# Performance work log

Hardware: AMD Instinct MI355X
Metric: run time of the kernel (lower is better)

## Reference

```python
import jax, jax.numpy as jnp
import numpy as np

VOXEL_DIM = (64, 64, 64)
VOXEL_SIZE = 0.04
STRIDE = 4.0  # backbone2d_stride


def setup_inputs() -> dict:
    key = jax.random.key(0)
    k1, k2 = jax.random.split(key, 2)
    bs, nv, cin, h, w = 4, 12, 384, 64, 64
    cout = 32
    vit_feats = jax.random.normal(k1, (bs, nv, cin, h, w), dtype=jnp.float32)
    w_reduce = jax.random.normal(k2, (cout, cin), dtype=jnp.float32) * 0.05
    b_reduce = jnp.zeros((cout,), dtype=jnp.float32)
    # Realistic pinhole projections: K @ [I | t], camera ~3m from grid center.
    rng = np.random.default_rng(0)
    f, cx, cy = 128.0, 128.0, 128.0
    K = np.array([[f, 0.0, cx], [0.0, f, cy], [0.0, 0.0, 1.0]])
    projs = np.zeros((bs, nv, 3, 4), dtype=np.float32)
    for v in range(nv):
        t = np.array([0.2 * rng.standard_normal(), 0.2 * rng.standard_normal(),
                      3.0 + 0.3 * rng.standard_normal()])
        E = np.concatenate([np.eye(3), t[:, None]], axis=1)  # 3x4
        projs[:, v] = (K @ E).astype(np.float32)
    return {"vit_feats": vit_feats, "w_reduce": w_reduce,
            "b_reduce": b_reduce, "projection": jnp.asarray(projs)}


def _backproject(proj, feats):
    """proj: (b,3,4), feats: (b,c,h,w) -> volume (b,c,N), valid (b,N)."""
    nx, ny, nz = VOXEL_DIM
    N = nx * ny * nz
    b, c, h, w = feats.shape
    X, Y, Z = jnp.meshgrid(jnp.arange(nx), jnp.arange(ny), jnp.arange(nz), indexing='ij')
    coords = jnp.stack([X.ravel(), Y.ravel(), Z.ravel()]).astype(feats.dtype)  # (3, N)
    origin = jnp.array([[-nx * VOXEL_SIZE / 2],
                        [-ny * VOXEL_SIZE / 2],
                        [-nz * VOXEL_SIZE / 2]], dtype=feats.dtype)
    world = coords * VOXEL_SIZE + origin                    # (3, N)
    world = jnp.concatenate([world, jnp.ones((1, N), feats.dtype)], axis=0)  # (4, N)
    cam = jnp.einsum('bij,jn->bin', proj, world)            # (b, 3, N)
    px = jnp.round(cam[:, 0] / cam[:, 2]).astype(jnp.int32)
    py = jnp.round(cam[:, 1] / cam[:, 2]).astype(jnp.int32)
    pz = cam[:, 2]
    valid = (px >= 0) & (py >= 0) & (px < w) & (py < h) & (pz > 0)  # (b, N)
    pxc = jnp.clip(px, 0, w - 1)
    pyc = jnp.clip(py, 0, h - 1)
    # per-batch gather: feats[b, :, py, px]
    gath = jax.vmap(lambda f, yy, xx: f[:, yy, xx])(feats, pyc, pxc)  # (b, c, N)
    vol = jnp.where(valid[:, None, :], gath, jnp.zeros((), feats.dtype))
    return vol, valid


def reference(vit_feats, w_reduce, b_reduce, projection):
    bs, nv, cin, h, w = vit_feats.shape
    cout = w_reduce.shape[0]
    nx, ny, nz = VOXEL_DIM
    N = nx * ny * nz
    # 1x1 conv channel reduction
    feats = jnp.einsum('bnchw,oc->bnohw', vit_feats, w_reduce) \
            + b_reduce[None, None, :, None, None]
    # divide intrinsics rows by the 2D backbone stride
    proj = projection.at[:, :, :2, :].set(projection[:, :, :2, :] / STRIDE)
    feats_v = jnp.moveaxis(feats, 1, 0)   # (nv, b, c, h, w)
    proj_v = jnp.moveaxis(proj, 1, 0)     # (nv, b, 3, 4)

    def step(carry, xs):
        vol, cnt = carry
        p, f = xs
        v, m = _backproject(p, f)
        return (vol + v, cnt + m.astype(vol.dtype)), None

    vol0 = jnp.zeros((bs, cout, N), jnp.float32)
    cnt0 = jnp.zeros((bs, N), jnp.float32)
    (vol, cnt), _ = jax.lax.scan(step, (vol0, cnt0), (proj_v, feats_v))
    # volume / valid, zeroed where never observed
    cnt_b = cnt[:, None, :]
    out = jnp.where(cnt_b > 0, vol / jnp.maximum(cnt_b, 1.0), jnp.zeros((), vol.dtype))
    return out.reshape(bs, cout, nx, ny, nz)
```

## Files before the change

kernel.cpp:

```cpp
#include <hip/hip_runtime.h>

#define NV 12
#define CIN 384
#define COUT 32
#define HW 4096
#define NVOX 262144
#define KSTEPS 12
#define KSTEP 32
#define KPAD 33
#define PIXB 64

typedef __attribute__((ext_vector_type(8))) short short8v;
typedef __attribute__((ext_vector_type(4))) short short4v;
typedef __attribute__((ext_vector_type(4))) float f32x4;

__device__ __forceinline__ short bf16b(float x) {
    union { float f; unsigned u; } c; c.f = x;
    unsigned r = (c.u + 0x7fffu + ((c.u >> 16) & 1u)) >> 16;
    return (short)r;
}

__global__ __launch_bounds__(256) void w_prep_kernel(
    const float* __restrict__ w, short* __restrict__ wfrag)
{
    const int t = blockIdx.x * 256 + threadIdx.x;
    if (t >= 48 * 32) return;
    const int sg = t >> 5, o = t & 31;
    const int s = sg >> 2, g = sg & 3;
    short8v v;
#pragma unroll
    for (int i = 0; i < 8; ++i)
        v[i] = bf16b(w[o * CIN + s * 32 + g * 8 + i]);
    *reinterpret_cast<short8v*>(wfrag + t * 8) = v;
}

__global__ __launch_bounds__(256) void mv_reduce_mfma_kernel(
    const float* __restrict__ vit, const short* __restrict__ wfrag,
    const float* __restrict__ bias, short* __restrict__ feats)
{
    __shared__ float lds[PIXB][KPAD];

    const int bid  = blockIdx.x;
    const int bv   = bid >> 6;
    const int pix0 = (bid & 63) * PIXB;

    const int tid  = threadIdx.x;
    const int wave = tid >> 6;
    const int l    = tid & 63;
    const int col  = l & 15;
    const int g    = l >> 4;

    const int kk  = tid >> 4;
    const int px4 = (tid & 15) * 4;

    const float* vbase = vit + (size_t)bv * CIN * HW + pix0;
    const short8v* wf  = reinterpret_cast<const short8v*>(wfrag);

    f32x4 acc0 = {0.f, 0.f, 0.f, 0.f};
    f32x4 acc1 = {0.f, 0.f, 0.f, 0.f};

#pragma unroll
    for (int s = 0; s < KSTEPS; ++s) {
        const float4 r0 = *reinterpret_cast<const float4*>(
            vbase + (size_t)(s * KSTEP + kk) * HW + px4);
        const float4 r1 = *reinterpret_cast<const float4*>(
            vbase + (size_t)(s * KSTEP + kk + 16) * HW + px4);

        __syncthreads();
        lds[px4 + 0][kk] = r0.x;  lds[px4 + 1][kk] = r0.y;
        lds[px4 + 2][kk] = r0.z;  lds[px4 + 3][kk] = r0.w;
        lds[px4 + 0][kk + 16] = r1.x;  lds[px4 + 1][kk + 16] = r1.y;
        lds[px4 + 2][kk + 16] = r1.z;  lds[px4 + 3][kk + 16] = r1.w;
        __syncthreads();

        const float4 f0 = *reinterpret_cast<const float4*>(&lds[wave * 16 + col][8 * g]);
        const float4 f1 = *reinterpret_cast<const float4*>(&lds[wave * 16 + col][8 * g + 4]);

        short8v bfr;
        bfr[0] = bf16b(f0.x); bfr[1] = bf16b(f0.y);
        bfr[2] = bf16b(f0.z); bfr[3] = bf16b(f0.w);
        bfr[4] = bf16b(f1.x); bfr[5] = bf16b(f1.y);
        bfr[6] = bf16b(f1.z); bfr[7] = bf16b(f1.w);

        const short8v a0 = wf[(s * 4 + g) * 32 + col];
        const short8v a1 = wf[(s * 4 + g) * 32 + 16 + col];

        acc0 = __builtin_amdgcn_mfma_f32_16x16x32_bf16(a0, bfr, acc0, 0, 0, 0);
        acc1 = __builtin_amdgcn_mfma_f32_16x16x32_bf16(a1, bfr, acc1, 0, 0, 0);
    }

    short* dst = feats + ((size_t)bv * HW + pix0 + wave * 16 + col) * COUT;
    const float4 b0 = *reinterpret_cast<const float4*>(bias + 4 * g);
    const float4 b1 = *reinterpret_cast<const float4*>(bias + 16 + 4 * g);
    short4v o0, o1;
    o0[0] = bf16b(acc0[0] + b0.x); o0[1] = bf16b(acc0[1] + b0.y);
    o0[2] = bf16b(acc0[2] + b0.z); o0[3] = bf16b(acc0[3] + b0.w);
    o1[0] = bf16b(acc1[0] + b1.x); o1[1] = bf16b(acc1[1] + b1.y);
    o1[2] = bf16b(acc1[2] + b1.z); o1[3] = bf16b(acc1[3] + b1.w);
    *reinterpret_cast<short4v*>(dst + 4 * g) = o0;
    *reinterpret_cast<short4v*>(dst + 16 + 4 * g) = o1;
}

__global__ __launch_bounds__(256) void mv_fuse_kernel(
    const unsigned short* __restrict__ feats, const float* __restrict__ proj,
    float* __restrict__ out)
{
    __shared__ double P[NV][12];

    const int tid = threadIdx.x;
    const unsigned gid = blockIdx.x * 256u + tid;
    const int b = gid >> 18;
    const int n = gid & (NVOX - 1);

    if (tid < NV * 12) {
        const int v = tid / 12, e = tid - v * 12;
        const int r = e >> 2;
        const float s = (r < 2) ? 0.25f : 1.0f;
        P[v][e] = (double)(proj[((b * NV + v) * 3 + r) * 4 + (e & 3)] * s);
    }
    __syncthreads();

    const int k = n & 63, j = (n >> 6) & 63, i = n >> 12;
    const double wx = (double)i * 0.04 - 1.28;
    const double wy = (double)j * 0.04 - 1.28;
    const double wz = (double)k * 0.04 - 1.28;

    float acc[COUT];
#pragma unroll
    for (int o = 0; o < COUT; ++o) acc[o] = 0.0f;
    int cnt = 0;

    const unsigned short* fb = feats + (size_t)b * NV * HW * COUT;

    for (int v = 0; v < NV; ++v) {
        const double* p = P[v];
        const double cz = p[8] * wx + p[9] * wy + p[10] * wz + p[11];
        if (!(cz > 0.0)) continue;
        const double cx = p[0] * wx + p[1] * wy + p[2] * wz + p[3];
        const double cy = p[4] * wx + p[5] * wy + p[6] * wz + p[7];
        const double rcz = 1.0 / cz;
        const double u = rint(cx * rcz);
        const double t = rint(cy * rcz);
        if (u < 0.0 || u > 63.0 || t < 0.0 || t > 63.0) continue;
        const int px = (int)u, py = (int)t;

        const uint4* s4 = reinterpret_cast<const uint4*>(
            fb + ((size_t)(v * HW + py * 64 + px)) * COUT);
        ++cnt;
#pragma unroll
        for (int q = 0; q < 4; ++q) {
            const uint4 u4 = s4[q];
            acc[q * 8 + 0] += __uint_as_float(u4.x << 16);
            acc[q * 8 + 1] += __uint_as_float(u4.x & 0xffff0000u);
            acc[q * 8 + 2] += __uint_as_float(u4.y << 16);
            acc[q * 8 + 3] += __uint_as_float(u4.y & 0xffff0000u);
            acc[q * 8 + 4] += __uint_as_float(u4.z << 16);
            acc[q * 8 + 5] += __uint_as_float(u4.z & 0xffff0000u);
            acc[q * 8 + 6] += __uint_as_float(u4.w << 16);
            acc[q * 8 + 7] += __uint_as_float(u4.w & 0xffff0000u);
        }
    }

    const float sc = (cnt > 0) ? (1.0f / (float)cnt) : 0.0f;
    float* ob = out + (size_t)b * COUT * NVOX + n;
#pragma unroll
    for (int o = 0; o < COUT; ++o)
        ob[(size_t)o * NVOX] = acc[o] * sc;
}

extern "C" void kernel_launch(void* const* d_in, const int* in_sizes, int n_in,
                              void* d_out, int out_size, void* d_ws, size_t ws_size,
                              hipStream_t stream) {
    const float* vit  = (const float*)d_in[0];
    const float* w    = (const float*)d_in[1];
    const float* bias = (const float*)d_in[2];
    const float* proj = (const float*)d_in[3];
    float* out = (float*)d_out;

    short* wfrag = (short*)d_ws;
    short* feats = (short*)((char*)d_ws + 48 * 32 * 8 * 2);

    w_prep_kernel<<<6, 256, 0, stream>>>(w, wfrag);

    mv_reduce_mfma_kernel<<<3072, 256, 0, stream>>>(vit, wfrag, bias, feats);

    mv_fuse_kernel<<<4096, 256, 0, stream>>>(
        (const unsigned short*)feats, proj, out);
}
```

Before: 130.9 us.

## Make fuse-kernel gathers branchless via zero row and software-prefetch next view

The fuse kernel now computes all twelve view offsets up front, sending invalid projections to a zero-filled sentinel row that the prep kernel writes, so no divergent branches are needed. The feature loads for the next view are issued before the current view is accumulated, so gather latency overlaps with the adds. In exchange every thread always performs twelve 64-byte gathers even for invalid views, and register pressure rises from the offset array and double-buffered uint4 values.

```diff
diff --git a/kernel.cpp b/kernel.cpp
--- a/kernel.cpp
+++ b/kernel.cpp
@@ -9,6 +9,7 @@
 #define KSTEP 32
 #define KPAD 33
 #define PIXB 64
+#define ZROW_U4 786432
 
 typedef __attribute__((ext_vector_type(8))) short short8v;
 typedef __attribute__((ext_vector_type(4))) short short4v;
@@ -21,17 +22,22 @@
 }
 
 __global__ __launch_bounds__(256) void w_prep_kernel(
-    const float* __restrict__ w, short* __restrict__ wfrag)
+    const float* __restrict__ w, short* __restrict__ wfrag,
+    short* __restrict__ feats)
 {
     const int t = blockIdx.x * 256 + threadIdx.x;
-    if (t >= 48 * 32) return;
-    const int sg = t >> 5, o = t & 31;
-    const int s = sg >> 2, g = sg & 3;
-    short8v v;
-#pragma unroll
-    for (int i = 0; i < 8; ++i)
-        v[i] = bf16b(w[o * CIN + s * 32 + g * 8 + i]);
-    *reinterpret_cast<short8v*>(wfrag + t * 8) = v;
+    if (t < 48 * 32) {
+        const int sg = t >> 5, o = t & 31;
+        const int s = sg >> 2, g = sg & 3;
+        short8v v;
+#pragma unroll
+        for (int i = 0; i < 8; ++i)
+            v[i] = bf16b(w[o * CIN + s * 32 + g * 8 + i]);
+        *reinterpret_cast<short8v*>(wfrag + t * 8) = v;
+    } else if (t >= 1536 && t < 1540) {
+        reinterpret_cast<uint4*>(feats)[ZROW_U4 + (t - 1536)] =
+            make_uint4(0u, 0u, 0u, 0u);
+    }
 }
 
 __global__ __launch_bounds__(256) void mv_reduce_mfma_kernel(
@@ -125,40 +131,54 @@
     const double wy = (double)j * 0.04 - 1.28;
     const double wz = (double)k * 0.04 - 1.28;
 
-    float acc[COUT];
-#pragma unroll
-    for (int o = 0; o < COUT; ++o) acc[o] = 0.0f;
+    int off[NV];
     int cnt = 0;
-
-    const unsigned short* fb = feats + (size_t)b * NV * HW * COUT;
-
+    const int bbase = b * (NV * HW * 4);
+#pragma unroll
     for (int v = 0; v < NV; ++v) {
         const double* p = P[v];
         const double cz = p[8] * wx + p[9] * wy + p[10] * wz + p[11];
-        if (!(cz > 0.0)) continue;
         const double cx = p[0] * wx + p[1] * wy + p[2] * wz + p[3];
         const double cy = p[4] * wx + p[5] * wy + p[6] * wz + p[7];
         const double rcz = 1.0 / cz;
         const double u = rint(cx * rcz);
         const double t = rint(cy * rcz);
-        if (u < 0.0 || u > 63.0 || t < 0.0 || t > 63.0) continue;
-        const int px = (int)u, py = (int)t;
-
-        const uint4* s4 = reinterpret_cast<const uint4*>(
-            fb + ((size_t)(v * HW + py * 64 + px)) * COUT);
-        ++cnt;
-#pragma unroll
-        for (int q = 0; q < 4; ++q) {
-            const uint4 u4 = s4[q];
-            acc[q * 8 + 0] += __uint_as_float(u4.x << 16);
-            acc[q * 8 + 1] += __uint_as_float(u4.x & 0xffff0000u);
-            acc[q * 8 + 2] += __uint_as_float(u4.y << 16);
-            acc[q * 8 + 3] += __uint_as_float(u4.y & 0xffff0000u);
-            acc[q * 8 + 4] += __uint_as_float(u4.z << 16);
-            acc[q * 8 + 5] += __uint_as_float(u4.z & 0xffff0000u);
-            acc[q * 8 + 6] += __uint_as_float(u4.w << 16);
-            acc[q * 8 + 7] += __uint_as_float(u4.w & 0xffff0000u);
+        const bool valid = (cz > 0.0) & (u >= 0.0) & (u <= 63.0) &
+                           (t >= 0.0) & (t <= 63.0);
+        const double uc = fmin(fmax(u, 0.0), 63.0);
+        const double tc = fmin(fmax(t, 0.0), 63.0);
+        const int pix = (int)uc + 64 * (int)tc;
+        off[v] = valid ? (bbase + (v * HW + pix) * 4) : ZROW_U4;
+        cnt += valid ? 1 : 0;
+    }
+
+    float acc[COUT];
+#pragma unroll
+    for (int o = 0; o < COUT; ++o) acc[o] = 0.0f;
+
+    const uint4* f4 = reinterpret_cast<const uint4*>(feats);
+    uint4 c0 = f4[off[0]], c1 = f4[off[0] + 1],
+          c2 = f4[off[0] + 2], c3 = f4[off[0] + 3];
+
+#pragma unroll
+    for (int v = 0; v < NV; ++v) {
+        uint4 n0 = c0, n1 = c1, n2 = c2, n3 = c3;
+        if (v + 1 < NV) {
+            const int o2 = off[v + 1];
+            n0 = f4[o2]; n1 = f4[o2 + 1]; n2 = f4[o2 + 2]; n3 = f4[o2 + 3];
         }
+#define ACC8(u4, base)                                          \
+        acc[base + 0] += __uint_as_float(u4.x << 16);           \
+        acc[base + 1] += __uint_as_float(u4.x & 0xffff0000u);   \
+        acc[base + 2] += __uint_as_float(u4.y << 16);           \
+        acc[base + 3] += __uint_as_float(u4.y & 0xffff0000u);   \
+        acc[base + 4] += __uint_as_float(u4.z << 16);           \
+        acc[base + 5] += __uint_as_float(u4.z & 0xffff0000u);   \
+        acc[base + 6] += __uint_as_float(u4.w << 16);           \
+        acc[base + 7] += __uint_as_float(u4.w & 0xffff0000u);
+        ACC8(c0, 0) ACC8(c1, 8) ACC8(c2, 16) ACC8(c3, 24)
+#undef ACC8
+        c0 = n0; c1 = n1; c2 = n2; c3 = n3;
     }
 
     const float sc = (cnt > 0) ? (1.0f / (float)cnt) : 0.0f;
@@ -180,7 +200,7 @@
     short* wfrag = (short*)d_ws;
     short* feats = (short*)((char*)d_ws + 48 * 32 * 8 * 2);
 
-    w_prep_kernel<<<6, 256, 0, stream>>>(w, wfrag);
+    w_prep_kernel<<<7, 256, 0, stream>>>(w, wfrag, feats);
 
     mv_reduce_mfma_kernel<<<3072, 256, 0, stream>>>(vit, wfrag, bias, feats);
 
```

Result: slower. 146.2 us (+11.7%).
